# Kernel optimization log

Measured on AMD Instinct MI355X. Metric: run time of the kernel, lower is better.

The kernel has to match this reference:

```python
import jax, jax.numpy as jnp
import numpy as np

# ---- Cl(3,0) Cayley table: blade order [1, e1, e2, e3, e12, e13, e23, e123] ----
_IDX2BM = [0, 1, 2, 4, 3, 5, 6, 7]
_BM2IDX = {b: i for i, b in enumerate(_IDX2BM)}

def _blade_mul(i, j):
    a, b = _IDX2BM[i], _IDX2BM[j]
    s, aa = 0, a >> 1
    while aa:
        s += bin(aa & b).count('1')
        aa >>= 1
    return _BM2IDX[a ^ b], (-1) ** s

_pairs = [(i, j) + _blade_mul(i, j) for i in range(8) for j in range(8) if i != j]
_pairs = [(i, j, k, s) for (i, j, k, s) in _pairs if k != i and k != j]
SRC_I = np.array([p[0] for p in _pairs])  # (42,)
SRC_J = np.array([p[1] for p in _pairs])
TGT   = np.array([p[2] for p in _pairs])
SIGN  = np.array([p[3] for p in _pairs], dtype=np.float32)

ROPE_THETA = 10000.0


def _rope_tables(T, D, dtype):
    inv_freq = 1.0 / (ROPE_THETA ** (jnp.arange(0, D, 2, dtype=jnp.float32) / D))
    freqs = jnp.arange(T, dtype=jnp.float32)[:, None] * inv_freq[None, :]  # (T, D/2)
    emb = jnp.concatenate([freqs, freqs], axis=-1)  # (T, D)
    return jnp.cos(emb).astype(dtype), jnp.sin(emb).astype(dtype)


def _rotate_half(x):
    x1, x2 = jnp.split(x, 2, axis=-1)
    return jnp.concatenate([-x2, x1], axis=-1)


def setup_inputs() -> dict:
    key = jax.random.key(0)
    k1, k2, k3 = jax.random.split(key, 3)
    B, T, N, D = 2, 2048, 8, 128
    d_model = N * D
    mv = jax.random.normal(k1, (B, T, N, D), dtype=jnp.float32)
    # nn.Linear weights, stored as (in, out) for x @ W; scaled like default init
    W_qkv = jax.random.normal(k2, (d_model, 3 * d_model), dtype=jnp.float32) / np.sqrt(d_model)
    W_o = jax.random.normal(k3, (d_model, d_model), dtype=jnp.float32) / np.sqrt(d_model)
    alpha = jnp.ones((8, 8), dtype=jnp.float32) * 0.01  # cayley_mix_init_scale
    return {"mv": mv, "W_qkv": W_qkv, "W_o": W_o, "alpha": alpha}


def reference(mv, W_qkv, W_o, alpha):
    B, T, N, D = mv.shape
    x_flat = mv.reshape(B, T, N * D)
    qkv = (x_flat @ W_qkv).reshape(B, T, 3, N, D)
    q, k, v = qkv[:, :, 0], qkv[:, :, 1], qkv[:, :, 2]  # (B, T, N, D)

    cos, sin = _rope_tables(T, D, mv.dtype)  # (T, D)
    cos = cos[None, :, None, :]
    sin = sin[None, :, None, :]
    q = q * cos + _rotate_half(q) * sin
    k = k * cos + _rotate_half(k) * sin

    # (B, N, T, D)
    q = q.transpose(0, 2, 1, 3)
    k = k.transpose(0, 2, 1, 3)
    v = v.transpose(0, 2, 1, 3)

    scale = 1.0 / jnp.sqrt(jnp.asarray(D, dtype=mv.dtype))
    scores = jnp.einsum('bntd,bnsd->bnts', q, k) * scale  # (B, N, T, T)
    causal = jnp.tril(jnp.ones((T, T), dtype=bool))
    scores = jnp.where(causal[None, None], scores, -jnp.inf)
    attn = jax.nn.softmax(scores, axis=-1)
    out = jnp.einsum('bnts,bnsd->bntd', attn, v)  # (B, N, T, D)

    out = out.transpose(0, 2, 1, 3).reshape(B, T, N * D)
    out = (out @ W_o).reshape(B, T, N, D)

    # Cayley cross-blade mixing
    si, sj, tgt = jnp.asarray(SRC_I), jnp.asarray(SRC_J), jnp.asarray(TGT)
    pair_w = alpha[si, sj] * jnp.asarray(SIGN)  # (42,)
    contrib = out[:, :, si, :] * out[:, :, sj, :] * pair_w[None, None, :, None]
    mixed = jnp.zeros_like(out).at[:, :, tgt, :].add(contrib)
    return out + mixed
```

## Files before the change

### kernel.cpp

```cpp
#include <hip/hip_runtime.h>
#include <stdint.h>


typedef __attribute__((ext_vector_type(8)))  __bf16 bf16x8;
typedef __attribute__((ext_vector_type(8)))  uint16_t u16x8;
typedef __attribute__((ext_vector_type(4)))  float  f32x4;

__device__ __forceinline__ uint16_t f2bf(float f) {
    uint32_t u = __float_as_uint(f);
    u += 0x7FFFu + ((u >> 16) & 1u);
    return (uint16_t)(u >> 16);
}
__device__ __forceinline__ float bf2f(uint16_t h) {
    return __uint_as_float(((uint32_t)h) << 16);
}

__device__ __forceinline__ void gload_lds16(const void* g, void* l) {
    __builtin_amdgcn_global_load_lds(
        (__attribute__((address_space(1))) void*)g,
        (__attribute__((address_space(3))) void*)l, 16, 0, 0);
}

__global__ __launch_bounds__(256) void k_prep(const float* __restrict__ mv,
                                              const float* __restrict__ Wqkv,
                                              const float* __restrict__ Wo,
                                              uint16_t* __restrict__ Xbf,
                                              uint16_t* __restrict__ Wqt,
                                              uint16_t* __restrict__ Wot,
                                              float* __restrict__ ct,
                                              float* __restrict__ st) {
    __shared__ uint16_t tile[64][65];
    const int bid = blockIdx.x;
    const int tid = threadIdx.x;
    if (bid < 4096) {
        int i = bid * 256 + tid;
        float4 v = ((const float4*)mv)[i];
        ((ushort4*)Xbf)[i] = make_ushort4(f2bf(v.x), f2bf(v.y), f2bf(v.z), f2bf(v.w));
    } else if (bid < 5120) {
        const float* W; uint16_t* Wt; int N, bx, by;
        if (bid < 4864) { W = Wqkv; Wt = Wqt; N = 3072;
                          int b2 = bid - 4096; bx = b2 % 48; by = b2 / 48; }
        else            { W = Wo;   Wt = Wot; N = 1024;
                          int b3 = bid - 4864; bx = b3 & 15; by = b3 >> 4; }
        const int k0 = by * 64, n0 = bx * 64;
        const int c = tid & 63, r4 = tid >> 6;
#pragma unroll
        for (int i = 0; i < 16; ++i) {
            int r = r4 + i * 4;
            tile[r][c] = f2bf(W[(size_t)(k0 + r) * N + n0 + c]);
        }
        __syncthreads();
#pragma unroll
        for (int i = 0; i < 16; ++i) {
            int r = r4 + i * 4;
            Wt[(size_t)(n0 + r) * 1024 + k0 + c] = tile[c][r];
        }
    } else {
        int i = (bid - 5120) * 256 + tid;
        int t = i >> 6, f = i & 63;
        float inv = expf(-(float)f * 0.14391156830441f);
        float ang = (float)t * inv;
        ct[i] = cosf(ang);
        st[i] = sinf(ang);
    }
}

__global__ __launch_bounds__(256) void k_gemmqkv(const uint16_t* __restrict__ A,
                                                 const uint16_t* __restrict__ Bt,
                                                 const float* __restrict__ ct,
                                                 const float* __restrict__ st,
                                                 uint16_t* __restrict__ Qr,
                                                 uint16_t* __restrict__ Kr,
                                                 uint16_t* __restrict__ Vt) {
    __shared__ __align__(16) char smem[33792];
    uint16_t* Atile = (uint16_t*)smem;
    uint16_t* Btile = (uint16_t*)(smem + 16384);
    const int lin = blockIdx.y * 24 + blockIdx.x;
    const int logical = (lin & 7) * 96 + (lin >> 3);
    const int bx = logical % 24;
    const int m0 = (logical / 24) << 7, n0 = bx << 7;
    const int sec = bx >> 3, head = bx & 7;
    const int tid = threadIdx.x;
    const int l = tid & 63, w = tid >> 6;
    const int lr = l & 15, lg = l >> 4;
    const int wm = (w >> 1) << 6, wn = (w & 1) << 6;
    const int K = 1024;

    f32x4 acc[4][4];
#pragma unroll
    for (int i = 0; i < 4; ++i)
#pragma unroll
        for (int j = 0; j < 4; ++j) acc[i][j] = (f32x4){0.f, 0.f, 0.f, 0.f};

    for (int kt = 0; kt < 16; ++kt) {
        const int k0 = kt << 6;
        __syncthreads();
#pragma unroll
        for (int c = 0; c < 8; ++c) {
            int idx = c * 256 + tid;
            if (idx < 1024) {
                int r = idx >> 3, c16 = idx & 7;
                int sc = c16 ^ (r & 7);
                gload_lds16(A + (size_t)(m0 + r) * K + k0 + sc * 8, Atile + idx * 8);
            } else {
                int i2 = idx - 1024;
                int r = i2 >> 3, c16 = i2 & 7;
                int sc = c16 ^ (r & 7);
                gload_lds16(Bt + (size_t)(n0 + r) * K + k0 + sc * 8, Btile + i2 * 8);
            }
        }
        __syncthreads();
#pragma unroll
        for (int kk = 0; kk < 2; ++kk) {
            bf16x8 af[4], bfv[4];
#pragma unroll
            for (int i = 0; i < 4; ++i) {
                int ra = wm + i * 16 + lr;
                af[i]  = *(const bf16x8*)((char*)Atile + ra * 128 +
                          ((kk * 64 + lg * 16) ^ ((ra & 7) << 4)));
                int rb = wn + i * 16 + lr;
                bfv[i] = *(const bf16x8*)((char*)Btile + rb * 128 +
                          ((kk * 64 + lg * 16) ^ ((rb & 7) << 4)));
            }
#pragma unroll
            for (int mi = 0; mi < 4; ++mi)
#pragma unroll
                for (int ni = 0; ni < 4; ++ni)
                    acc[mi][ni] = __builtin_amdgcn_mfma_f32_16x16x32_bf16(
                        af[mi], bfv[ni], acc[mi][ni], 0, 0, 0);
        }
    }

    __syncthreads();
    uint16_t (*Tl)[132] = (uint16_t(*)[132])smem;
#pragma unroll
    for (int mi = 0; mi < 4; ++mi)
#pragma unroll
        for (int ni = 0; ni < 4; ++ni)
#pragma unroll
            for (int r = 0; r < 4; ++r)
                Tl[wm + mi * 16 + lg * 4 + r][wn + ni * 16 + lr] =
                    f2bf(acc[mi][ni][r]);
    __syncthreads();

    const int b = m0 >> 11, t0 = m0 & 2047;
    const size_t hidx = (size_t)(b * 8 + head);
    if (sec < 2) {
        uint16_t* outp = (sec == 0 ? Qr : Kr) + (hidx * 2048 + t0) * 128;
#pragma unroll
        for (int it = 0; it < 8; ++it) {
            int lin2 = it * 256 + tid;
            int tr = lin2 >> 4, d0 = (lin2 & 15) * 4;
            ushort4 lo = *(const ushort4*)&Tl[tr][d0];
            ushort4 hi = *(const ushort4*)&Tl[tr][d0 + 64];
            float4 cv = *(const float4*)&ct[(size_t)(t0 + tr) * 64 + d0];
            float4 sv = *(const float4*)&st[(size_t)(t0 + tr) * 64 + d0];
            ushort4 o1, o2;
            o1.x = f2bf(bf2f(lo.x) * cv.x - bf2f(hi.x) * sv.x);
            o2.x = f2bf(bf2f(hi.x) * cv.x + bf2f(lo.x) * sv.x);
            o1.y = f2bf(bf2f(lo.y) * cv.y - bf2f(hi.y) * sv.y);
            o2.y = f2bf(bf2f(hi.y) * cv.y + bf2f(lo.y) * sv.y);
            o1.z = f2bf(bf2f(lo.z) * cv.z - bf2f(hi.z) * sv.z);
            o2.z = f2bf(bf2f(hi.z) * cv.z + bf2f(lo.z) * sv.z);
            o1.w = f2bf(bf2f(lo.w) * cv.w - bf2f(hi.w) * sv.w);
            o2.w = f2bf(bf2f(hi.w) * cv.w + bf2f(lo.w) * sv.w);
            *(ushort4*)&outp[(size_t)tr * 128 + d0]      = o1;
            *(ushort4*)&outp[(size_t)tr * 128 + d0 + 64] = o2;
        }
    } else {
        uint16_t* vp = Vt + hidx * 128 * 2048;
#pragma unroll
        for (int it = 0; it < 8; ++it) {
            int lin2 = it * 256 + tid;
            int d = lin2 >> 4, tq = (lin2 & 15) * 8;
            ushort4 v0 = make_ushort4(Tl[tq + 0][d], Tl[tq + 1][d],
                                      Tl[tq + 2][d], Tl[tq + 3][d]);
            ushort4 v1 = make_ushort4(Tl[tq + 4][d], Tl[tq + 5][d],
                                      Tl[tq + 6][d], Tl[tq + 7][d]);
            *(ushort4*)&vp[(size_t)d * 2048 + t0 + tq]     = v0;
            *(ushort4*)&vp[(size_t)d * 2048 + t0 + tq + 4] = v1;
        }
    }
}

__global__ __launch_bounds__(256) void k_gemm2s(const uint16_t* __restrict__ A,
                                                const uint16_t* __restrict__ Bt,
                                                float* __restrict__ C) {
    __shared__ uint16_t Atile[128 * 64];
    __shared__ uint16_t Btile[64 * 64];
    const int kz = blockIdx.z;
    A  += (size_t)kz * 512;
    Bt += (size_t)kz * 512;
    C  += (size_t)kz * (4096u * 1024u);
    const int lin = blockIdx.y * 16 + blockIdx.x;
    const int logical = (lin & 7) * 64 + (lin >> 3);
    const int m0 = (logical >> 4) << 7, n0 = (logical & 15) << 6;
    const int tid = threadIdx.x;
    const int l = tid & 63, w = tid >> 6;
    const int lr = l & 15, lg = l >> 4;
    const int wm = (w >> 1) << 6, wn = (w & 1) << 5;

    f32x4 acc[4][2];
#pragma unroll
    for (int i = 0; i < 4; ++i)
#pragma unroll
        for (int j = 0; j < 2; ++j) acc[i][j] = (f32x4){0.f, 0.f, 0.f, 0.f};

    for (int kt = 0; kt < 8; ++kt) {
        const int k0 = kt << 6;
        __syncthreads();
#pragma unroll
        for (int c = 0; c < 6; ++c) {
            int idx = c * 256 + tid;
            if (idx < 1024) {
                int r = idx >> 3, c16 = idx & 7;
                int sc = c16 ^ (r & 7);
                gload_lds16(A + (size_t)(m0 + r) * 1024 + k0 + sc * 8, Atile + idx * 8);
            } else {
                int i2 = idx - 1024;
                int r = i2 >> 3, c16 = i2 & 7;
                int sc = c16 ^ (r & 7);
                gload_lds16(Bt + (size_t)(n0 + r) * 1024 + k0 + sc * 8, Btile + i2 * 8);
            }
        }
        __syncthreads();
#pragma unroll
        for (int kk = 0; kk < 2; ++kk) {
            bf16x8 af[4], bfv[2];
#pragma unroll
            for (int i = 0; i < 4; ++i) {
                int ra = wm + i * 16 + lr;
                af[i] = *(const bf16x8*)((char*)Atile + ra * 128 +
                         ((kk * 64 + lg * 16) ^ ((ra & 7) << 4)));
            }
#pragma unroll
            for (int j = 0; j < 2; ++j) {
                int rb = wn + j * 16 + lr;
                bfv[j] = *(const bf16x8*)((char*)Btile + rb * 128 +
                          ((kk * 64 + lg * 16) ^ ((rb & 7) << 4)));
            }
#pragma unroll
            for (int mi = 0; mi < 4; ++mi)
#pragma unroll
                for (int ni = 0; ni < 2; ++ni)
                    acc[mi][ni] = __builtin_amdgcn_mfma_f32_16x16x32_bf16(
                        af[mi], bfv[ni], acc[mi][ni], 0, 0, 0);
        }
    }
#pragma unroll
    for (int mi = 0; mi < 4; ++mi)
#pragma unroll
        for (int ni = 0; ni < 2; ++ni)
#pragma unroll
            for (int r = 0; r < 4; ++r) {
                int row = m0 + wm + mi * 16 + lg * 4 + r;
                int col = n0 + wn + ni * 16 + lr;
                C[(size_t)row * 1024 + col] = acc[mi][ni][r];
            }
}

__global__ __launch_bounds__(256) void k_attn(const uint16_t* __restrict__ Qg,
                                              const uint16_t* __restrict__ Kg,
                                              const uint16_t* __restrict__ Vtg,
                                              uint16_t* __restrict__ pbuf,
                                              float* __restrict__ mlg,
                                              uint16_t* __restrict__ AOg) {
    __shared__ uint16_t Klds[64 * 128];
    __shared__ uint16_t Vlds[128 * 64];
    __shared__ uint16_t Plds[4][16 * 64];

    const int h = blockIdx.x;
    int sy = blockIdx.y, qt = 31, ci = 0;
    for (int q = 31; q >= 0; --q) {
        int nc = (q + 8) >> 3;
        if (sy < nc) { qt = q; ci = sy; break; }
        sy -= nc;
    }
    const int slot = h * 80 + blockIdx.y;
    const int p0 = ci * 8;
    const int pend = min(p0 + 8, qt + 1);
    const int q0 = qt * 64;
    const int tid = threadIdx.x;
    const int l = tid & 63, w = tid >> 6;
    const int lr = l & 15, lg = l >> 4;
    const size_t headTD = (size_t)h * (2048 * 128);
    const uint16_t* Kh = Kg + headTD;
    const uint16_t* Vh = Vtg + headTD;

    bf16x8 qf[4];
    {
        const uint16_t* qp = Qg + headTD + (size_t)(q0 + w * 16 + lr) * 128 + lg * 8;
#pragma unroll
        for (int kc = 0; kc < 4; ++kc) qf[kc] = *(const bf16x8*)(qp + kc * 32);
    }

    f32x4 accO[8];
#pragma unroll
    for (int i = 0; i < 8; ++i) accO[i] = (f32x4){0.f, 0.f, 0.f, 0.f};
    float mrun = -1e30f, lrun = 0.f;

    const float SL2E = 0.08838834764831845f * 1.4426950408889634f;
    const int   swz  = (lr & 7) << 4;
    uint16_t* Pw = &Plds[w][0];

    auto STAGE = [&](int k0) {
#pragma unroll
        for (int p = 0; p < 4; ++p) {
            int u = p * 256 + tid;
            int row = u >> 4;
            int c16 = (u & 15) ^ (row & 7);
            gload_lds16(Kh + (size_t)(k0 + row) * 128 + c16 * 8,
                        (char*)&Klds[0] + u * 16);
        }
#pragma unroll
        for (int p = 0; p < 4; ++p) {
            int u = p * 256 + tid;
            int d = u >> 3;
            int c8 = (u & 7) ^ (d & 7);
            gload_lds16(Vh + (size_t)d * 2048 + k0 + c8 * 8,
                        (char*)&Vlds[0] + u * 16);
        }
    };

    for (int kt = p0; kt < pend; ++kt) {
        STAGE(kt * 64);
        asm volatile("s_waitcnt vmcnt(0)" ::: "memory");
        __builtin_amdgcn_s_barrier();
        __builtin_amdgcn_sched_barrier(0);

        const char* Kb = (const char*)&Klds[0];
        const char* Vb = (const char*)&Vlds[0];

        float sv[4][4];
        __builtin_amdgcn_s_setprio(1);
#pragma unroll
        for (int cg = 0; cg < 4; ++cg) {
            f32x4 a = (f32x4){0.f, 0.f, 0.f, 0.f};
#pragma unroll
            for (int kc = 0; kc < 4; ++kc) {
                int kb = (cg * 16 + lr) * 256 + ((kc * 64 + lg * 16) ^ swz);
                bf16x8 kf = *(const bf16x8*)(Kb + kb);
                a = __builtin_amdgcn_mfma_f32_16x16x32_bf16(kf, qf[kc], a, 0, 0, 0);
            }
#pragma unroll
            for (int r = 0; r < 4; ++r) sv[cg][r] = a[r];
        }
        __builtin_amdgcn_s_setprio(0);

        if (kt == qt) {
#pragma unroll
            for (int cg = 0; cg < 4; ++cg)
#pragma unroll
                for (int r = 0; r < 4; ++r)
                    if (cg * 16 + lg * 4 + r > w * 16 + lr) sv[cg][r] = -1e30f;
        }

        float pml = sv[0][0];
#pragma unroll
        for (int cg = 0; cg < 4; ++cg)
#pragma unroll
            for (int r = 0; r < 4; ++r) pml = fmaxf(pml, sv[cg][r]);

        if (!__all(pml * SL2E <= mrun + 11.f)) {
            float mx = pml;
            mx = fmaxf(mx, __shfl_xor(mx, 16, 64));
            mx = fmaxf(mx, __shfl_xor(mx, 32, 64));
            float mn = fmaxf(mrun, mx * SL2E);
            float corr = exp2f(mrun - mn);
            mrun = mn;
            lrun *= corr;
            float ca[4];
#pragma unroll
            for (int r = 0; r < 4; ++r)
                ca[r] = __shfl(corr, (lg << 4) + lg * 4 + r, 64);
#pragma unroll
            for (int i = 0; i < 8; ++i)
#pragma unroll
                for (int r = 0; r < 4; ++r) accO[i][r] *= ca[r];
        }

        float psum = 0.f;
        float p[4][4];
#pragma unroll
        for (int cg = 0; cg < 4; ++cg)
#pragma unroll
            for (int r = 0; r < 4; ++r) {
                p[cg][r] = exp2f(fmaf(sv[cg][r], SL2E, -mrun));
                psum += p[cg][r];
            }
        lrun += psum;

#pragma unroll
        for (int cg = 0; cg < 4; ++cg) {
            uint32_t w0, w1;
            asm("v_cvt_pk_bf16_f32 %0, %1, %2" : "=v"(w0) : "v"(p[cg][0]), "v"(p[cg][1]));
            asm("v_cvt_pk_bf16_f32 %0, %1, %2" : "=v"(w1) : "v"(p[cg][2]), "v"(p[cg][3]));
            uint2 pr; pr.x = w0; pr.y = w1;
            *(uint2*)((char*)Pw + lr * 128 + ((cg * 32 + lg * 8) ^ swz)) = pr;
        }

        asm volatile("" ::: "memory");
        bf16x8 pf[2];
#pragma unroll
        for (int c = 0; c < 2; ++c)
            pf[c] = *(const bf16x8*)((char*)Pw + lr * 128 + ((c * 64 + lg * 16) ^ swz));

        __builtin_amdgcn_s_setprio(1);
#pragma unroll
        for (int ni = 0; ni < 8; ++ni)
#pragma unroll
            for (int c = 0; c < 2; ++c) {
                int vb = (ni * 16 + lr) * 128 + ((c * 64 + lg * 16) ^ swz);
                bf16x8 vf = *(const bf16x8*)(Vb + vb);
                accO[ni] = __builtin_amdgcn_mfma_f32_16x16x32_bf16(pf[c], vf, accO[ni], 0, 0, 0);
            }
        __builtin_amdgcn_s_setprio(0);

        __builtin_amdgcn_s_barrier();
    }

    float lsum = lrun;
    lsum += __shfl_xor(lsum, 16, 64);
    lsum += __shfl_xor(lsum, 32, 64);

    if (qt <= 7) {
        float linv = 1.f / lsum;
        float inv[4];
#pragma unroll
        for (int r = 0; r < 4; ++r)
            inv[r] = __shfl(linv, (lg << 4) + lg * 4 + r, 64);
        const int b = h >> 3, n = h & 7;
#pragma unroll
        for (int ni = 0; ni < 8; ++ni)
#pragma unroll
            for (int r = 0; r < 4; ++r) {
                int trow = q0 + w * 16 + lg * 4 + r;
                AOg[((size_t)(b * 2048 + trow)) * 1024 + n * 128 + ni * 16 + lr] =
                    f2bf(accO[ni][r] * inv[r]);
            }
    } else {
        uint16_t* pb = pbuf + (size_t)slot * 8192;
#pragma unroll
        for (int ni = 0; ni < 8; ++ni)
#pragma unroll
            for (int r = 0; r < 4; ++r) {
                int row = w * 16 + lg * 4 + r;
                pb[row * 128 + ni * 16 + lr] = f2bf(accO[ni][r]);
            }
        if (lg == 0) {
            mlg[slot * 128 + w * 16 + lr]      = mrun;
            mlg[slot * 128 + 64 + w * 16 + lr] = lsum;
        }
    }
}

__global__ __launch_bounds__(256) void k_amerge(const uint16_t* __restrict__ pbuf,
                                                const float* __restrict__ mlg,
                                                uint16_t* __restrict__ AOg) {
    const int h = blockIdx.x, qt = 8 + blockIdx.y;
    int base = 0;
    for (int q = 31; q > qt; --q) base += (q + 8) >> 3;
    const int nc = (qt + 8) >> 3;
    const int slot0 = h * 80 + base;
    const int tid = threadIdx.x;
    const int row = tid >> 2, dq = (tid & 3) * 32;

    float M = -1e30f;
    for (int ci = 0; ci < nc; ++ci)
        M = fmaxf(M, mlg[(slot0 + ci) * 128 + row]);
    float L = 0.f;
    float o[32];
#pragma unroll
    for (int j = 0; j < 32; ++j) o[j] = 0.f;
    for (int ci = 0; ci < nc; ++ci) {
        int sl = slot0 + ci;
        float wgt = exp2f(mlg[sl * 128 + row] - M);
        L += mlg[sl * 128 + 64 + row] * wgt;
        const u16x8* pv = (const u16x8*)(pbuf + (size_t)sl * 8192 + row * 128 + dq);
#pragma unroll
        for (int jj = 0; jj < 4; ++jj) {
            u16x8 v = pv[jj];
#pragma unroll
            for (int k = 0; k < 8; ++k) o[jj * 8 + k] += bf2f(v[k]) * wgt;
        }
    }
    float inv = 1.f / L;
    const int b = h >> 3, n = h & 7;
    uint16_t* op = AOg + ((size_t)(b * 2048 + qt * 64 + row)) * 1024 + n * 128 + dq;
#pragma unroll
    for (int jj = 0; jj < 4; ++jj) {
        u16x8 v;
#pragma unroll
        for (int k = 0; k < 8; ++k) v[k] = f2bf(o[jj * 8 + k] * inv);
        ((u16x8*)op)[jj] = v;
    }
}

__global__ __launch_bounds__(256) void k_mix(const float* __restrict__ out0,
                                             const float* __restrict__ out1,
                                             const float* __restrict__ alpha,
                                             float* __restrict__ fin) {
    constexpr int SI[42] = {1,1,1,1,1,1, 2,2,2,2,2,2, 3,3,3,3,3,3, 4,4,4,4,4,4,
                            5,5,5,5,5,5, 6,6,6,6,6,6, 7,7,7,7,7,7};
    constexpr int SJ[42] = {2,3,4,5,6,7, 1,3,4,5,6,7, 1,2,4,5,6,7, 1,2,3,5,6,7,
                            1,2,3,4,6,7, 1,2,3,4,5,7, 1,2,3,4,5,6};
    constexpr int TG[42] = {4,5,2,3,7,6, 4,6,1,7,3,5, 5,6,7,1,2,4, 2,1,7,6,5,3,
                            3,7,1,6,4,2, 7,3,2,5,4,1, 6,5,4,3,2,1};
    constexpr float SG[42] = {+1,+1,+1,+1,+1,+1, -1,+1,-1,-1,+1,-1, -1,-1,+1,-1,-1,+1,
                              -1,+1,+1,-1,+1,-1, -1,-1,+1,+1,-1,+1, +1,-1,+1,-1,+1,-1,
                              +1,-1,+1,-1,+1,-1};
    int idx = blockIdx.x * 256 + threadIdx.x;
    int dq = (idx & 31) * 4, bt = idx >> 5;
    size_t base = (size_t)bt * 1024 + dq;
    float4 o[8], r[8];
#pragma unroll
    for (int hh = 0; hh < 8; ++hh) {
        float4 a = *(const float4*)&out0[base + hh * 128];
        float4 b = *(const float4*)&out1[base + hh * 128];
        o[hh] = make_float4(a.x + b.x, a.y + b.y, a.z + b.z, a.w + b.w);
        r[hh] = o[hh];
    }
#pragma unroll
    for (int p = 0; p < 42; ++p) {
        float wgt = alpha[SI[p] * 8 + SJ[p]] * SG[p];
        r[TG[p]].x += wgt * o[SI[p]].x * o[SJ[p]].x;
        r[TG[p]].y += wgt * o[SI[p]].y * o[SJ[p]].y;
        r[TG[p]].z += wgt * o[SI[p]].z * o[SJ[p]].z;
        r[TG[p]].w += wgt * o[SI[p]].w * o[SJ[p]].w;
    }
#pragma unroll
    for (int hh = 0; hh < 8; ++hh) *(float4*)&fin[base + hh * 128] = r[hh];
}

extern "C" void kernel_launch(void* const* d_in, const int* in_sizes, int n_in,
                              void* d_out, int out_size, void* d_ws, size_t ws_size,
                              hipStream_t stream) {
    (void)in_sizes; (void)n_in; (void)out_size; (void)ws_size;
    const float* mv    = (const float*)d_in[0];
    const float* Wqkv  = (const float*)d_in[1];
    const float* Wo    = (const float*)d_in[2];
    const float* alpha = (const float*)d_in[3];
    float* outp = (float*)d_out;
    char* ws = (char*)d_ws;

    uint16_t* Xbf  = (uint16_t*)(ws + 0);
    uint16_t* Wqt  = (uint16_t*)(ws + 8388608);
    uint16_t* Wot  = (uint16_t*)(ws + 14680064);
    uint16_t* Qr   = (uint16_t*)(ws + 41943040);
    uint16_t* Kr   = (uint16_t*)(ws + 50331648);
    uint16_t* Vt   = (uint16_t*)(ws + 58720256);
    float*    ctab = (float*)(ws + 67108864);
    float*    stab = (float*)(ws + 67633152);
    uint16_t* AO   = (uint16_t*)(ws + 0);
    float*    mlg  = (float*)(ws + 8388608);
    uint16_t* pbuf = (uint16_t*)(ws + 16777216);
    float*    outF0 = (float*)(ws + 16777216);
    float*    outF1 = (float*)(ws + 33554432);

    k_prep   <<<5632, 256, 0, stream>>>(mv, Wqkv, Wo, Xbf, Wqt, Wot, ctab, stab);
    k_gemmqkv<<<dim3(24, 32), 256, 0, stream>>>(Xbf, Wqt, ctab, stab, Qr, Kr, Vt);
    k_attn   <<<dim3(16, 80), 256, 0, stream>>>(Qr, Kr, Vt, pbuf, mlg, AO);
    k_amerge <<<dim3(16, 24), 256, 0, stream>>>(pbuf, mlg, AO);
    k_gemm2s <<<dim3(16, 32, 2), 256, 0, stream>>>(AO, Wot, outF0);
    k_mix    <<<512, 256, 0, stream>>>(outF0, outF1, alpha, outp);
}
```

Baseline: 120.3 us.

## Double-buffer K/V tiles in attention with 32-key tiles and prefetch

Shrinks the attention key tile from 64 to 32 rows and adds a second LDS buffer for K and V. The next tile's global-to-LDS loads are issued right after the barrier, so memory latency overlaps the current tile's MFMA and softmax work. The trailing barrier is removed and the causal mask is generalised to the finer tiles. Each tile now does half the MFMA work per barrier and online-softmax step, which adds per-iteration overhead, and removing the barrier risks WAR hazards on the P buffer and the K/V double buffer.

```diff
diff --git a/kernel.cpp b/kernel.cpp
--- a/kernel.cpp
+++ b/kernel.cpp
@@ -265,9 +265,9 @@
                                               uint16_t* __restrict__ pbuf,
                                               float* __restrict__ mlg,
                                               uint16_t* __restrict__ AOg) {
-    __shared__ uint16_t Klds[64 * 128];
-    __shared__ uint16_t Vlds[128 * 64];
-    __shared__ uint16_t Plds[4][16 * 64];
+    __shared__ uint16_t Klds[2][32 * 128];
+    __shared__ uint16_t Vlds[2][128 * 32];
+    __shared__ uint16_t Plds[4][16 * 32];
 
     const int h = blockIdx.x;
     int sy = blockIdx.y, qt = 31, ci = 0;
@@ -277,8 +277,8 @@
         sy -= nc;
     }
     const int slot = h * 80 + blockIdx.y;
-    const int p0 = ci * 8;
-    const int pend = min(p0 + 8, qt + 1);
+    const int p0   = ci * 16;
+    const int pend = min(p0 + 16, 2 * qt + 2);
     const int q0 = qt * 64;
     const int tid = threadIdx.x;
     const int l = tid & 63, w = tid >> 6;
@@ -300,45 +300,48 @@
     float mrun = -1e30f, lrun = 0.f;
 
     const float SL2E = 0.08838834764831845f * 1.4426950408889634f;
-    const int   swz  = (lr & 7) << 4;
+    const int swzK = (lr & 7) << 4;
+    const int swzP = (lr & 3) << 4;
     uint16_t* Pw = &Plds[w][0];
 
-    auto STAGE = [&](int k0) {
-#pragma unroll
-        for (int p = 0; p < 4; ++p) {
+    auto STAGE = [&](int buf, int kt) {
+        const int k0 = kt * 32;
+#pragma unroll
+        for (int p = 0; p < 2; ++p) {
             int u = p * 256 + tid;
             int row = u >> 4;
             int c16 = (u & 15) ^ (row & 7);
             gload_lds16(Kh + (size_t)(k0 + row) * 128 + c16 * 8,
-                        (char*)&Klds[0] + u * 16);
-        }
-#pragma unroll
-        for (int p = 0; p < 4; ++p) {
+                        (char*)&Klds[buf][0] + u * 16);
+        }
+#pragma unroll
+        for (int p = 0; p < 2; ++p) {
             int u = p * 256 + tid;
-            int d = u >> 3;
-            int c8 = (u & 7) ^ (d & 7);
-            gload_lds16(Vh + (size_t)d * 2048 + k0 + c8 * 8,
-                        (char*)&Vlds[0] + u * 16);
+            int d = u >> 2, c4 = u & 3;
+            gload_lds16(Vh + (size_t)d * 2048 + k0 + (c4 ^ (d & 3)) * 8,
+                        (char*)&Vlds[buf][0] + u * 16);
         }
     };
 
+    STAGE(0, p0);
+
     for (int kt = p0; kt < pend; ++kt) {
-        STAGE(kt * 64);
         asm volatile("s_waitcnt vmcnt(0)" ::: "memory");
         __builtin_amdgcn_s_barrier();
         __builtin_amdgcn_sched_barrier(0);
-
-        const char* Kb = (const char*)&Klds[0];
-        const char* Vb = (const char*)&Vlds[0];
-
-        float sv[4][4];
+        if (kt + 1 < pend) STAGE((kt + 1) & 1, kt + 1);
+
+        const char* Kb = (const char*)&Klds[kt & 1][0];
+        const char* Vb = (const char*)&Vlds[kt & 1][0];
+
+        float sv[2][4];
         __builtin_amdgcn_s_setprio(1);
 #pragma unroll
-        for (int cg = 0; cg < 4; ++cg) {
+        for (int cg = 0; cg < 2; ++cg) {
             f32x4 a = (f32x4){0.f, 0.f, 0.f, 0.f};
 #pragma unroll
             for (int kc = 0; kc < 4; ++kc) {
-                int kb = (cg * 16 + lr) * 256 + ((kc * 64 + lg * 16) ^ swz);
+                int kb = (cg * 16 + lr) * 256 + ((kc * 64 + lg * 16) ^ swzK);
                 bf16x8 kf = *(const bf16x8*)(Kb + kb);
                 a = __builtin_amdgcn_mfma_f32_16x16x32_bf16(kf, qf[kc], a, 0, 0, 0);
             }
@@ -347,17 +350,19 @@
         }
         __builtin_amdgcn_s_setprio(0);
 
-        if (kt == qt) {
-#pragma unroll
-            for (int cg = 0; cg < 4; ++cg)
+        if (kt >= 2 * qt) {
+            int qg = w * 16 + lr;
+            int kbase = kt * 32 - q0;
+#pragma unroll
+            for (int cg = 0; cg < 2; ++cg)
 #pragma unroll
                 for (int r = 0; r < 4; ++r)
-                    if (cg * 16 + lg * 4 + r > w * 16 + lr) sv[cg][r] = -1e30f;
+                    if (kbase + cg * 16 + lg * 4 + r > qg) sv[cg][r] = -1e30f;
         }
 
         float pml = sv[0][0];
 #pragma unroll
-        for (int cg = 0; cg < 4; ++cg)
+        for (int cg = 0; cg < 2; ++cg)
 #pragma unroll
             for (int r = 0; r < 4; ++r) pml = fmaxf(pml, sv[cg][r]);
 
@@ -380,9 +385,9 @@
         }
 
         float psum = 0.f;
-        float p[4][4];
-#pragma unroll
-        for (int cg = 0; cg < 4; ++cg)
+        float p[2][4];
+#pragma unroll
+        for (int cg = 0; cg < 2; ++cg)
 #pragma unroll
             for (int r = 0; r < 4; ++r) {
                 p[cg][r] = exp2f(fmaf(sv[cg][r], SL2E, -mrun));
@@ -391,32 +396,25 @@
         lrun += psum;
 
 #pragma unroll
-        for (int cg = 0; cg < 4; ++cg) {
+        for (int cg = 0; cg < 2; ++cg) {
             uint32_t w0, w1;
             asm("v_cvt_pk_bf16_f32 %0, %1, %2" : "=v"(w0) : "v"(p[cg][0]), "v"(p[cg][1]));
             asm("v_cvt_pk_bf16_f32 %0, %1, %2" : "=v"(w1) : "v"(p[cg][2]), "v"(p[cg][3]));
             uint2 pr; pr.x = w0; pr.y = w1;
-            *(uint2*)((char*)Pw + lr * 128 + ((cg * 32 + lg * 8) ^ swz)) = pr;
+            *(uint2*)((char*)Pw + lr * 64 + ((cg * 32 + lg * 8) ^ swzP)) = pr;
         }
 
         asm volatile("" ::: "memory");
-        bf16x8 pf[2];
-#pragma unroll
-        for (int c = 0; c < 2; ++c)
-            pf[c] = *(const bf16x8*)((char*)Pw + lr * 128 + ((c * 64 + lg * 16) ^ swz));
+        bf16x8 pf = *(const bf16x8*)((char*)Pw + lr * 64 + ((lg * 16) ^ swzP));
 
         __builtin_amdgcn_s_setprio(1);
 #pragma unroll
-        for (int ni = 0; ni < 8; ++ni)
-#pragma unroll
-            for (int c = 0; c < 2; ++c) {
-                int vb = (ni * 16 + lr) * 128 + ((c * 64 + lg * 16) ^ swz);
-                bf16x8 vf = *(const bf16x8*)(Vb + vb);
-                accO[ni] = __builtin_amdgcn_mfma_f32_16x16x32_bf16(pf[c], vf, accO[ni], 0, 0, 0);
-            }
+        for (int ni = 0; ni < 8; ++ni) {
+            int vb = (ni * 16 + lr) * 64 + ((lg * 16) ^ swzP);
+            bf16x8 vf = *(const bf16x8*)(Vb + vb);
+            accO[ni] = __builtin_amdgcn_mfma_f32_16x16x32_bf16(pf, vf, accO[ni], 0, 0, 0);
+        }
         __builtin_amdgcn_s_setprio(0);
-
-        __builtin_amdgcn_s_barrier();
     }
 
     float lsum = lrun;
```

Result: slower. 126.5 us (+5.2%).
